# Optimization experiments

Hardware: AMD Instinct MI355X
Metric: run time of the kernel (lower is better)

Reference implementation:

```python
import jax, jax.numpy as jnp
import numpy as np

N, S, I, L, M = 4096, 8, 256, 512, 256


def setup_inputs() -> dict:
    key = jax.random.key(0)
    ks = jax.random.split(key, 13)
    sc_in = 1.0 / np.sqrt(I + L)
    sc_out = 1.0 / np.sqrt(L)
    return {
        "modulation": jax.random.normal(ks[0], (N, S * I), jnp.float32),
        "h0": jax.random.normal(ks[1], (N, S * L), jnp.float32),
        "c0": jax.random.normal(ks[2], (N, S * L), jnp.float32),
        "Wi": jax.random.normal(ks[3], (S, L, I + L), jnp.float32) * sc_in,
        "bi": jnp.full((S, L), -1.0, jnp.float32),  # init_input bias
        "Wf": jax.random.normal(ks[4], (S, L, I + L), jnp.float32) * sc_in,
        "bf": jnp.full((S, L), 1.0, jnp.float32),   # init_forget bias
        "Wg": jax.random.normal(ks[5], (S, L, I + L), jnp.float32) * sc_in,
        "bg": jnp.zeros((S, L), jnp.float32),
        "Wo": jax.random.normal(ks[6], (S, L, I + L), jnp.float32) * sc_in,
        "bo": jnp.zeros((S, L), jnp.float32),
        "Wy": jax.random.normal(ks[7], (S, M, L), jnp.float32) * sc_out,
        "by": jnp.zeros((S, M), jnp.float32),
    }


def reference(modulation, h0, c0, Wi, bi, Wf, bf, Wg, bg, Wo, bo, Wy, by):
    n = modulation.shape[0]
    x = modulation.reshape(n, S, I)          # [N,S,I]
    h = h0.reshape(n, S, L)                  # [N,S,L]
    c = c0.reshape(n, S, L)
    xh = jnp.concatenate([x, h], axis=-1)    # cat_groups: per-stream [x_s, h_s] -> [N,S,I+L]
    # grouped per-stream linear projections for the four gates
    i = jax.nn.sigmoid(jnp.einsum('nsd,sld->nsl', xh, Wi) + bi)
    f = jax.nn.sigmoid(jnp.einsum('nsd,sld->nsl', xh, Wf) + bf)
    g = jnp.tanh(jnp.einsum('nsd,sld->nsl', xh, Wg) + bg)
    o = jax.nn.sigmoid(jnp.einsum('nsd,sld->nsl', xh, Wo) + bo)
    c_new = f * c + i * g
    h_new = o * jnp.tanh(c_new)              # dropout p=0 -> identity
    y = jnp.einsum('nsl,sml->nsm', h_new, Wy) + by
    return y.reshape(n, S * M)
```

## Files before the change

### kernel.cpp

```cpp
#include <hip/hip_runtime.h>
#include <stdint.h>

#define S_ 8
#define N_ 4096
#define I_ 256
#define L_ 512
#define M_ 256
#define D_ 768
#define NT64 12

typedef __bf16 bf16x8 __attribute__((ext_vector_type(8)));
typedef float f32x4 __attribute__((ext_vector_type(4)));
typedef unsigned short ushort_t;

__device__ __forceinline__ unsigned short f2bf(float f) {
  union { float f; uint32_t u; } c; c.f = f;
  uint32_t u = c.u;
  uint32_t r = u + 0x7FFFu + ((u >> 16) & 1u);
  return (unsigned short)(r >> 16);
}

__device__ __forceinline__ float fsigmoid(float x) {
  return 1.0f / (1.0f + __expf(-x));
}
__device__ __forceinline__ float ftanh(float x) {
  float ax = fabsf(x);
  float e = __expf(-2.0f * ax);
  float t = (1.0f - e) / (1.0f + e);
  return copysignf(t, x);
}

#define GLD16(gsrc, ldst)                                                                  \
  __builtin_amdgcn_global_load_lds(                                                        \
      (const __attribute__((address_space(1))) uint32_t*)(uintptr_t)(gsrc),                \
      (__attribute__((address_space(3))) uint32_t*)(uintptr_t)(ldst), 16, 0, 0)

__global__ __launch_bounds__(256) void prep_kernel(
    const float* __restrict__ mod, const float* __restrict__ h0,
    const float* __restrict__ Wi, const float* __restrict__ Wf,
    const float* __restrict__ Wg, const float* __restrict__ Wo,
    const float* __restrict__ Wy, ushort_t* __restrict__ w4,
    ushort_t* __restrict__ wyb, ushort_t* __restrict__ xh) {
  const int y = blockIdx.y;
  int t = blockIdx.x * 256 + threadIdx.x;
  const int stride = gridDim.x * 256;
  if (y < 4) {
    const float* src = (y == 0) ? Wi : (y == 1) ? Wf : (y == 2) ? Wg : Wo;
    ushort_t* dst = w4 + (size_t)y * S_ * L_ * D_;
    const int n4 = S_ * L_ * D_ / 4;
    for (; t < n4; t += stride) {
      float4 v = ((const float4*)src)[t];
      ushort4 o;
      o.x = f2bf(v.x); o.y = f2bf(v.y); o.z = f2bf(v.z); o.w = f2bf(v.w);
      ((ushort4*)dst)[t] = o;
    }
  } else if (y == 4) {
    const int n4 = S_ * M_ * L_ / 4;
    for (; t < n4; t += stride) {
      float4 v = ((const float4*)Wy)[t];
      ushort4 o;
      o.x = f2bf(v.x); o.y = f2bf(v.y); o.z = f2bf(v.z); o.w = f2bf(v.w);
      ((ushort4*)wyb)[t] = o;
    }
  } else if (y == 5) {
    const int total = S_ * N_ * (I_ / 4);
    for (; t < total; t += stride) {
      int r = t >> 6, c = t & 63;
      int s = r >> 12, n = r & (N_ - 1);
      float4 v = *(const float4*)(mod + (size_t)n * (S_ * I_) + s * I_ + c * 4);
      ushort4 o;
      o.x = f2bf(v.x); o.y = f2bf(v.y); o.z = f2bf(v.z); o.w = f2bf(v.w);
      *(ushort4*)(xh + (size_t)r * D_ + c * 4) = o;
    }
  } else {
    const int total = S_ * N_ * (L_ / 4);
    for (; t < total; t += stride) {
      int r = t >> 7, c = t & 127;
      int s = r >> 12, n = r & (N_ - 1);
      float4 v = *(const float4*)(h0 + (size_t)n * (S_ * L_) + s * L_ + c * 4);
      ushort4 o;
      o.x = f2bf(v.x); o.y = f2bf(v.y); o.z = f2bf(v.z); o.w = f2bf(v.w);
      *(ushort4*)(xh + (size_t)r * D_ + I_ + c * 4) = o;
    }
  }
}

__global__ __launch_bounds__(1024, 4) void gates_kernel(
    const ushort_t* __restrict__ xh,
    const ushort_t* __restrict__ w4,
    const float* __restrict__ bi, const float* __restrict__ bff,
    const float* __restrict__ bg, const float* __restrict__ bo,
    const float* __restrict__ c0,
    ushort_t* __restrict__ hout)
{
  __shared__ __align__(16) ushort_t smem[65536];
  const int tid = threadIdx.x;
  const int lane = tid & 63;
  const int ln15 = lane & 15;
  const int ln4 = lane >> 4;
  const int w = tid >> 6;
  const int wm = w >> 2;
  const int wl = w & 3;

  const int bid = blockIdx.x;
  const int s = bid & 7;
  const int r = bid >> 3;
  const int n0 = (r >> 3) << 8;
  const int l0 = (r & 7) << 6;

  const size_t xh_base = (size_t)(s * N_ + n0) * D_;

  const ushort_t* aSrc[2];
  const ushort_t* bSrc[2];
  #pragma unroll
  for (int rd = 0; rd < 2; ++rd) {
    int slot = tid + (rd << 10);
    int row = slot >> 3;
    int cg = (slot & 7) ^ (row & 7);
    aSrc[rd] = xh + xh_base + (size_t)row * D_ + (cg << 3);
    int g = row >> 6, ll = row & 63;
    bSrc[rd] = w4 + ((size_t)((g * S_ + s) * L_) + l0 + ll) * D_ + (cg << 3);
  }

#define STAGE(base, tile) do {                                                          \
    const int k0_ = (tile) << 6;                                                        \
    GLD16(aSrc[0] + k0_, &smem[((base) + (w << 6)) * 8]);                               \
    GLD16(aSrc[1] + k0_, &smem[((base) + 1024 + (w << 6)) * 8]);                        \
    GLD16(bSrc[0] + k0_, &smem[((base) + 2048 + (w << 6)) * 8]);                        \
    GLD16(bSrc[1] + k0_, &smem[((base) + 3072 + (w << 6)) * 8]);                        \
  } while (0)

  const char* smemB = (const char*)smem;
  const uint32_t chk0 = (uint32_t)((ln4 ^ (ln15 & 7)) << 4);
  const uint32_t chk1 = (uint32_t)(((4 + ln4) ^ (ln15 & 7)) << 4);
  const uint32_t aBase = (uint32_t)(((wm << 6) + ln15) << 7);
  const uint32_t bBase = 32768u + (uint32_t)(((wl << 4) + ln15) << 7);
  const uint32_t aK0 = aBase + chk0, aK1 = aBase + chk1;
  const uint32_t bK0 = bBase + chk0, bK1 = bBase + chk1;

  f32x4 acc[4][4];
  #pragma unroll
  for (int i = 0; i < 4; ++i)
    #pragma unroll
    for (int j = 0; j < 4; ++j) {
      f32x4 z = {0.f, 0.f, 0.f, 0.f};
      acc[i][j] = z;
    }

#define COMPUTE(pA, pB) do {                                                            \
    bf16x8 a_[4], b_[4];                                                                \
    _Pragma("unroll")                                                                   \
    for (int rt_ = 0; rt_ < 4; ++rt_) a_[rt_] = *(const bf16x8*)((pA) + rt_ * 2048);    \
    _Pragma("unroll")                                                                   \
    for (int g_ = 0; g_ < 4; ++g_) b_[g_] = *(const bf16x8*)((pB) + g_ * 8192);         \
    _Pragma("unroll")                                                                   \
    for (int rt_ = 0; rt_ < 4; ++rt_)                                                   \
      _Pragma("unroll")                                                                 \
      for (int g_ = 0; g_ < 4; ++g_)                                                    \
        acc[rt_][g_] = __builtin_amdgcn_mfma_f32_16x16x32_bf16(                         \
            a_[rt_], b_[g_], acc[rt_][g_], 0, 0, 0);                                    \
  } while (0)

  STAGE(0, 0);
  asm volatile("s_waitcnt vmcnt(0)" ::: "memory");
  __syncthreads();

  #pragma unroll 1
  for (int t = 0; t < NT64; ++t) {
    const int cur = (t & 1) << 12;
    const uint32_t curB = (uint32_t)(t & 1) << 16;
    if (t + 1 < NT64) STAGE(cur ^ 4096, t + 1);

    const char* pA0 = smemB + (aK0 + curB);
    const char* pA1 = smemB + (aK1 + curB);
    const char* pB0 = smemB + (bK0 + curB);
    const char* pB1 = smemB + (bK1 + curB);

    if (w & 1) {
      COMPUTE(pA1, pB1);
      COMPUTE(pA0, pB0);
    } else {
      COMPUTE(pA0, pB0);
      COMPUTE(pA1, pB1);
    }

    asm volatile("s_waitcnt vmcnt(0)" ::: "memory");
    __syncthreads();
  }

  const int l = l0 + (wl << 4) + ln15;
  const float vbi = bi[s * L_ + l];
  const float vbf = bff[s * L_ + l];
  const float vbg = bg[s * L_ + l];
  const float vbo = bo[s * L_ + l];
  #pragma unroll
  for (int rt = 0; rt < 4; ++rt) {
    #pragma unroll
    for (int j = 0; j < 4; ++j) {
      const int n = n0 + (wm << 6) + (rt << 4) + (ln4 << 2) + j;
      const float c0v = c0[(size_t)n * (S_ * L_) + s * L_ + l];
      const float iv = fsigmoid(acc[rt][0][j] + vbi);
      const float fv = fsigmoid(acc[rt][1][j] + vbf);
      const float gv = ftanh(acc[rt][2][j] + vbg);
      const float ov = fsigmoid(acc[rt][3][j] + vbo);
      const float cn = fv * c0v + iv * gv;
      const float hn = ov * ftanh(cn);
      hout[(size_t)(s * N_ + n) * L_ + l] = f2bf(hn);
    }
  }
#undef STAGE
#undef COMPUTE
}

__global__ __launch_bounds__(256, 2) void out_kernel(
    const ushort_t* __restrict__ h,
    const ushort_t* __restrict__ wy,
    const float* __restrict__ by,
    float* __restrict__ out)
{
  __shared__ __align__(16) ushort_t smem[1536 * 8];
  const int tid = threadIdx.x;
  const int lane = tid & 63;
  const int w = tid >> 6;
  const int n0 = blockIdx.x * 128;
  const int m0 = blockIdx.y * 64;
  const int s = blockIdx.z;

  f32x4 acc[2][4];
  #pragma unroll
  for (int rt = 0; rt < 2; ++rt)
    #pragma unroll
    for (int ct = 0; ct < 4; ++ct) {
      f32x4 z = {0.f, 0.f, 0.f, 0.f};
      acc[rt][ct] = z;
    }

  const size_t h_row0 = (size_t)(s * N_ + n0) * L_;

  for (int t = 0; t < L_ / 64; ++t) {
    const int k0 = t * 64;
    #pragma unroll
    for (int it = 0; it < 4; ++it) {
      int chunk = it * 256 + tid;
      int rr = chunk >> 3, c = chunk & 7;
      int cg = c ^ (rr & 7);
      const ushort_t* src = h + h_row0 + (size_t)rr * L_ + k0 + cg * 8;
      GLD16(src, &smem[(it * 256 + w * 64) * 8]);
    }
    #pragma unroll
    for (int it = 0; it < 2; ++it) {
      int chunk = it * 256 + tid;
      int rl = chunk >> 3, c = chunk & 7;
      int cg = c ^ (rl & 7);
      const ushort_t* src = wy + ((size_t)(s * M_ + m0 + rl)) * L_ + k0 + cg * 8;
      GLD16(src, &smem[(1024 + it * 256 + w * 64) * 8]);
    }
    __syncthreads();
    #pragma unroll
    for (int kk = 0; kk < 2; ++kk) {
      const int cc = kk * 4 + (lane >> 4);
      bf16x8 av[2];
      #pragma unroll
      for (int rt = 0; rt < 2; ++rt) {
        int rr = w * 32 + rt * 16 + (lane & 15);
        av[rt] = *(const bf16x8*)&smem[(rr * 8 + (cc ^ (rr & 7))) * 8];
      }
      #pragma unroll
      for (int ct = 0; ct < 4; ++ct) {
        int rl = ct * 16 + (lane & 15);
        bf16x8 b = *(const bf16x8*)&smem[(1024 + rl * 8 + (cc ^ (rl & 7))) * 8];
        acc[0][ct] = __builtin_amdgcn_mfma_f32_16x16x32_bf16(av[0], b, acc[0][ct], 0, 0, 0);
        acc[1][ct] = __builtin_amdgcn_mfma_f32_16x16x32_bf16(av[1], b, acc[1][ct], 0, 0, 0);
      }
    }
    __syncthreads();
  }

  #pragma unroll
  for (int ct = 0; ct < 4; ++ct) {
    const int m = m0 + ct * 16 + (lane & 15);
    const float vb = by[s * M_ + m];
    #pragma unroll
    for (int rt = 0; rt < 2; ++rt) {
      #pragma unroll
      for (int j = 0; j < 4; ++j) {
        const int n = n0 + w * 32 + rt * 16 + (lane >> 4) * 4 + j;
        out[(size_t)n * (S_ * M_) + s * M_ + m] = acc[rt][ct][j] + vb;
      }
    }
  }
}


extern "C" void kernel_launch(void* const* d_in, const int* in_sizes, int n_in,
                              void* d_out, int out_size, void* d_ws, size_t ws_size,
                              hipStream_t stream) {
  const float* mod = (const float*)d_in[0];
  const float* h0  = (const float*)d_in[1];
  const float* c0  = (const float*)d_in[2];
  const float* Wi  = (const float*)d_in[3];
  const float* bi  = (const float*)d_in[4];
  const float* Wf  = (const float*)d_in[5];
  const float* bf  = (const float*)d_in[6];
  const float* Wg  = (const float*)d_in[7];
  const float* bg  = (const float*)d_in[8];
  const float* Wo  = (const float*)d_in[9];
  const float* bo  = (const float*)d_in[10];
  const float* Wy  = (const float*)d_in[11];
  const float* by  = (const float*)d_in[12];
  float* out = (float*)d_out;

  ushort_t* ws = (ushort_t*)d_ws;
  ushort_t* xh   = ws;
  ushort_t* w4   = xh  + (size_t)S_ * N_ * D_;
  ushort_t* wyb  = w4  + (size_t)4 * S_ * L_ * D_;
  ushort_t* hbuf = wyb + (size_t)S_ * M_ * L_;

  prep_kernel<<<dim3(768, 7), 256, 0, stream>>>(mod, h0, Wi, Wf, Wg, Wo, Wy, w4, wyb, xh);
  gates_kernel<<<1024, 1024, 0, stream>>>(xh, w4, bi, bf, bg, bo, c0, hbuf);
  out_kernel<<<dim3(N_ / 128, M_ / 64, S_), 256, 0, stream>>>(hbuf, wyb, by, out);
}
```

Before: 200.3 us.

## Halve gates-kernel waves with larger per-wave tiles; remap out_kernel grid

```diff
diff --git a/kernel.cpp b/kernel.cpp
--- a/kernel.cpp
+++ b/kernel.cpp
@@ -85,7 +85,7 @@
   }
 }
 
-__global__ __launch_bounds__(1024, 4) void gates_kernel(
+__global__ __launch_bounds__(512, 2) void gates_kernel(
     const ushort_t* __restrict__ xh,
     const ushort_t* __restrict__ w4,
     const float* __restrict__ bi, const float* __restrict__ bff,
@@ -99,8 +99,8 @@
   const int ln15 = lane & 15;
   const int ln4 = lane >> 4;
   const int w = tid >> 6;
-  const int wm = w >> 2;
-  const int wl = w & 3;
+  const int wm = w >> 1;
+  const int wl = w & 1;
 
   const int bid = blockIdx.x;
   const int s = bid & 7;
@@ -110,11 +110,11 @@
 
   const size_t xh_base = (size_t)(s * N_ + n0) * D_;
 
-  const ushort_t* aSrc[2];
-  const ushort_t* bSrc[2];
-  #pragma unroll
-  for (int rd = 0; rd < 2; ++rd) {
-    int slot = tid + (rd << 10);
+  const ushort_t* aSrc[4];
+  const ushort_t* bSrc[4];
+  #pragma unroll
+  for (int rd = 0; rd < 4; ++rd) {
+    int slot = tid + (rd << 9);
     int row = slot >> 3;
     int cg = (slot & 7) ^ (row & 7);
     aSrc[rd] = xh + xh_base + (size_t)row * D_ + (cg << 3);
@@ -124,46 +124,50 @@
 
 #define STAGE(base, tile) do {                                                          \
     const int k0_ = (tile) << 6;                                                        \
-    GLD16(aSrc[0] + k0_, &smem[((base) + (w << 6)) * 8]);                               \
-    GLD16(aSrc[1] + k0_, &smem[((base) + 1024 + (w << 6)) * 8]);                        \
-    GLD16(bSrc[0] + k0_, &smem[((base) + 2048 + (w << 6)) * 8]);                        \
-    GLD16(bSrc[1] + k0_, &smem[((base) + 3072 + (w << 6)) * 8]);                        \
+    _Pragma("unroll")                                                                   \
+    for (int rd_ = 0; rd_ < 4; ++rd_) {                                                 \
+      GLD16(aSrc[rd_] + k0_, &smem[((base) + (rd_ << 9) + (w << 6)) * 8]);              \
+      GLD16(bSrc[rd_] + k0_, &smem[((base) + 2048 + (rd_ << 9) + (w << 6)) * 8]);       \
+    }                                                                                   \
   } while (0)
 
   const char* smemB = (const char*)smem;
   const uint32_t chk0 = (uint32_t)((ln4 ^ (ln15 & 7)) << 4);
   const uint32_t chk1 = (uint32_t)(((4 + ln4) ^ (ln15 & 7)) << 4);
   const uint32_t aBase = (uint32_t)(((wm << 6) + ln15) << 7);
-  const uint32_t bBase = 32768u + (uint32_t)(((wl << 4) + ln15) << 7);
+  const uint32_t bBase = 32768u + (uint32_t)(((wl << 5) + ln15) << 7);
   const uint32_t aK0 = aBase + chk0, aK1 = aBase + chk1;
   const uint32_t bK0 = bBase + chk0, bK1 = bBase + chk1;
 
-  f32x4 acc[4][4];
+  f32x4 acc[4][8];
   #pragma unroll
   for (int i = 0; i < 4; ++i)
     #pragma unroll
-    for (int j = 0; j < 4; ++j) {
+    for (int j = 0; j < 8; ++j) {
       f32x4 z = {0.f, 0.f, 0.f, 0.f};
       acc[i][j] = z;
     }
 
-#define COMPUTE(pA, pB) do {                                                            \
-    bf16x8 a_[4], b_[4];                                                                \
+  STAGE(0, 0);
+  asm volatile("s_waitcnt vmcnt(0)" ::: "memory");
+  __syncthreads();
+
+#define KKSTEP(pA, pB) do {                                                             \
+    bf16x8 a_[4], b_[8];                                                                \
     _Pragma("unroll")                                                                   \
     for (int rt_ = 0; rt_ < 4; ++rt_) a_[rt_] = *(const bf16x8*)((pA) + rt_ * 2048);    \
     _Pragma("unroll")                                                                   \
-    for (int g_ = 0; g_ < 4; ++g_) b_[g_] = *(const bf16x8*)((pB) + g_ * 8192);         \
+    for (int g_ = 0; g_ < 4; ++g_) {                                                    \
+      b_[(g_ << 1) + 0] = *(const bf16x8*)((pB) + g_ * 8192);                           \
+      b_[(g_ << 1) + 1] = *(const bf16x8*)((pB) + g_ * 8192 + 2048);                    \
+    }                                                                                   \
     _Pragma("unroll")                                                                   \
     for (int rt_ = 0; rt_ < 4; ++rt_)                                                   \
       _Pragma("unroll")                                                                 \
-      for (int g_ = 0; g_ < 4; ++g_)                                                    \
-        acc[rt_][g_] = __builtin_amdgcn_mfma_f32_16x16x32_bf16(                         \
-            a_[rt_], b_[g_], acc[rt_][g_], 0, 0, 0);                                    \
+      for (int cj_ = 0; cj_ < 8; ++cj_)                                                 \
+        acc[rt_][cj_] = __builtin_amdgcn_mfma_f32_16x16x32_bf16(                        \
+            a_[rt_], b_[cj_], acc[rt_][cj_], 0, 0, 0);                                  \
   } while (0)
-
-  STAGE(0, 0);
-  asm volatile("s_waitcnt vmcnt(0)" ::: "memory");
-  __syncthreads();
 
   #pragma unroll 1
   for (int t = 0; t < NT64; ++t) {
@@ -171,45 +175,38 @@
     const uint32_t curB = (uint32_t)(t & 1) << 16;
     if (t + 1 < NT64) STAGE(cur ^ 4096, t + 1);
 
-    const char* pA0 = smemB + (aK0 + curB);
-    const char* pA1 = smemB + (aK1 + curB);
-    const char* pB0 = smemB + (bK0 + curB);
-    const char* pB1 = smemB + (bK1 + curB);
-
-    if (w & 1) {
-      COMPUTE(pA1, pB1);
-      COMPUTE(pA0, pB0);
-    } else {
-      COMPUTE(pA0, pB0);
-      COMPUTE(pA1, pB1);
-    }
+    KKSTEP(smemB + (aK0 + curB), smemB + (bK0 + curB));
+    KKSTEP(smemB + (aK1 + curB), smemB + (bK1 + curB));
 
     asm volatile("s_waitcnt vmcnt(0)" ::: "memory");
     __syncthreads();
   }
 
-  const int l = l0 + (wl << 4) + ln15;
-  const float vbi = bi[s * L_ + l];
-  const float vbf = bff[s * L_ + l];
-  const float vbg = bg[s * L_ + l];
-  const float vbo = bo[s * L_ + l];
-  #pragma unroll
-  for (int rt = 0; rt < 4; ++rt) {
-    #pragma unroll
-    for (int j = 0; j < 4; ++j) {
-      const int n = n0 + (wm << 6) + (rt << 4) + (ln4 << 2) + j;
-      const float c0v = c0[(size_t)n * (S_ * L_) + s * L_ + l];
-      const float iv = fsigmoid(acc[rt][0][j] + vbi);
-      const float fv = fsigmoid(acc[rt][1][j] + vbf);
-      const float gv = ftanh(acc[rt][2][j] + vbg);
-      const float ov = fsigmoid(acc[rt][3][j] + vbo);
-      const float cn = fv * c0v + iv * gv;
-      const float hn = ov * ftanh(cn);
-      hout[(size_t)(s * N_ + n) * L_ + l] = f2bf(hn);
+  #pragma unroll
+  for (int ct = 0; ct < 2; ++ct) {
+    const int l = l0 + (wl << 5) + (ct << 4) + ln15;
+    const float vbi = bi[s * L_ + l];
+    const float vbf = bff[s * L_ + l];
+    const float vbg = bg[s * L_ + l];
+    const float vbo = bo[s * L_ + l];
+    #pragma unroll
+    for (int rt = 0; rt < 4; ++rt) {
+      #pragma unroll
+      for (int j = 0; j < 4; ++j) {
+        const int n = n0 + (wm << 6) + (rt << 4) + (ln4 << 2) + j;
+        const float c0v = c0[(size_t)n * (S_ * L_) + s * L_ + l];
+        const float iv = fsigmoid(acc[rt][0 + ct][j] + vbi);
+        const float fv = fsigmoid(acc[rt][2 + ct][j] + vbf);
+        const float gv = ftanh(acc[rt][4 + ct][j] + vbg);
+        const float ov = fsigmoid(acc[rt][6 + ct][j] + vbo);
+        const float cn = fv * c0v + iv * gv;
+        const float hn = ov * ftanh(cn);
+        hout[(size_t)(s * N_ + n) * L_ + l] = f2bf(hn);
+      }
     }
   }
 #undef STAGE
-#undef COMPUTE
+#undef KKSTEP
 }
 
 __global__ __launch_bounds__(256, 2) void out_kernel(
@@ -222,9 +219,12 @@
   const int tid = threadIdx.x;
   const int lane = tid & 63;
   const int w = tid >> 6;
-  const int n0 = blockIdx.x * 128;
-  const int m0 = blockIdx.y * 64;
-  const int s = blockIdx.z;
+
+  const int bid = blockIdx.x;
+  const int s = bid & 7;
+  const int r = bid >> 3;
+  const int n0 = (r >> 2) << 7;
+  const int m0 = (r & 3) << 6;
 
   f32x4 acc[2][4];
   #pragma unroll
@@ -317,6 +317,6 @@
   ushort_t* hbuf = wyb + (size_t)S_ * M_ * L_;
 
   prep_kernel<<<dim3(768, 7), 256, 0, stream>>>(mod, h0, Wi, Wf, Wg, Wo, Wy, w4, wyb, xh);
-  gates_kernel<<<1024, 1024, 0, stream>>>(xh, w4, bi, bf, bg, bo, c0, hbuf);
-  out_kernel<<<dim3(N_ / 128, M_ / 64, S_), 256, 0, stream>>>(hbuf, wyb, by, out);
-}
+  gates_kernel<<<1024, 512, 0, stream>>>(xh, w4, bi, bf, bg, bo, c0, hbuf);
+  out_kernel<<<1024, 256, 0, stream>>>(hbuf, wyb, by, out);
+}
```

New measurement: 199.5 us. Within noise of the previous version (-0.4%).
